# Kernel optimization log

Hardware: AMD Instinct MI355X
Metric: run time of the kernel (lower is better)

Reference implementation:

```python
import jax, jax.numpy as jnp
import numpy as np

N_NODES = 100000
N_EDGES = 1600000
F_IN = 16
F_OUT = 16
N_BASIS = 4  # per spatial dim; basisTerms = [4, 4]


def linear_basis(u, n):
    """Piecewise-linear (hat) basis, n terms on [-1, 1]. u: [E] -> [E, n]."""
    centers = jnp.linspace(-1.0, 1.0, n, dtype=u.dtype)
    dx = 2.0 / (n - 1)
    return jnp.maximum(0.0, 1.0 - jnp.abs(u[:, None] - centers[None, :]) / dx)


def setup_inputs() -> dict:
    key = jax.random.key(0)
    k1, k2, k3, k4, k5 = jax.random.split(key, 5)
    x = jax.random.normal(k1, (N_NODES, F_IN), dtype=jnp.float32)
    edge_index = jax.random.randint(k2, (2, N_EDGES), 0, N_NODES, dtype=jnp.int64)
    # relative positions normalized to [-1, 1]^2 (as in initializeWeights2D)
    edge_attr = jax.random.uniform(k3, (N_EDGES, 2), dtype=jnp.float32,
                                   minval=-1.0, maxval=1.0)
    # weight: [*basisTerms, inputFeatures, outputFeatures], uniform(-0.05, 0.05)
    weight = jax.random.uniform(k4, (N_BASIS, N_BASIS, F_IN, F_OUT),
                                dtype=jnp.float32, minval=-0.05, maxval=0.05)
    return {"x": x, "edge_index": edge_index, "edge_attr": edge_attr,
            "weight": weight}


def reference(x, edge_index, edge_attr, weight):
    """BasisConvLayer forward, mode='conv', linear basis, no bias/activations.

    For each edge e=(i<-j): msg_e = sum_{u,v} b_u(dx) b_v(dy) * (x_j @ W[u,v]);
    out[i] = sum over incoming edges of msg_e.
    """
    row, col = edge_index[0], edge_index[1]
    x_j = x[col]                                   # [E, F_in] gather
    bx = linear_basis(edge_attr[:, 0], N_BASIS)    # [E, nB]
    by = linear_basis(edge_attr[:, 1], N_BASIS)    # [E, nB]
    # outer product of 1D bases -> [E, nB*nB] interpolation coefficients
    t = (bx[:, :, None] * by[:, None, :]).reshape(-1, N_BASIS * N_BASIS)
    w_flat = weight.reshape(N_BASIS * N_BASIS, F_IN, F_OUT)
    # accumulate over the small fixed basis-term set to avoid [E, Fin, Fout]
    msg = jnp.zeros((x_j.shape[0], F_OUT), dtype=x.dtype)
    for k in range(N_BASIS * N_BASIS):
        msg = msg + t[:, k, None] * (x_j @ w_flat[k])
    out = jax.ops.segment_sum(msg, row, num_segments=N_NODES)  # scatter-add
    return out
```

## Files before the change

kernel.cpp:

```cpp
#include <hip/hip_runtime.h>

#define N_NODES 100000
#define N_EDGES 1600000
#define F 16

#define EDGES_PER_BLOCK 512
#define ITERS 4

#define OUT_FLOAT4 ((N_NODES * F) / 4)

typedef __attribute__((ext_vector_type(8))) short bf16x8;
typedef __attribute__((ext_vector_type(4))) float f32x4;

__global__ __launch_bounds__(256) void zero_out_kernel(float4* __restrict__ out) {
    int i = blockIdx.x * 256 + threadIdx.x;
    if (i < OUT_FLOAT4) out[i] = make_float4(0.f, 0.f, 0.f, 0.f);
}

__device__ __forceinline__ unsigned pk_bf16(float lo, float hi) {
    unsigned r;
    asm("v_cvt_pk_bf16_f32 %0, %1, %2" : "=v"(r) : "v"(lo), "v"(hi));
    return r;
}

__global__ __launch_bounds__(256, 4) void basis_conv_mfma(
    const float* __restrict__ x,
    const int*   __restrict__ edge_index,
    const float* __restrict__ edge_attr,
    const float* __restrict__ weight,
    float*       __restrict__ out)
{
    const int lane = threadIdx.x & 63;
    const int wid  = threadIdx.x >> 6;
    const int e15  = lane & 15;
    const int fo   = lane & 15;
    const int c    = lane >> 4;
    const int hv   = c >> 1;
    const int i0   = (c & 1) * 8;

    bf16x8 bw[8];
#pragma unroll
    for (int m = 0; m < 8; ++m) {
        const float* wp = weight + (2 * m + hv) * 256 + i0 * 16 + fo;
        union { bf16x8 v; unsigned w[4]; } bb;
#pragma unroll
        for (int p = 0; p < 4; ++p)
            bb.w[p] = pk_bf16(wp[(2 * p) * 16], wp[(2 * p + 1) * 16]);
        bw[m] = bb.v;
    }

    const int wbase = blockIdx.x * EDGES_PER_BLOCK + wid * (32 * ITERS);

    float2 at0[2], at1[2];
    int    col1[2];
    float4 xa0[2], xb0[2];

    {
#pragma unroll
        for (int u = 0; u < 2; ++u) {
            const int egA = wbase + u * 16;
            const int col0 = edge_index[N_EDGES + egA + e15];
            at0[u] = ((const float2*)edge_attr)[egA + e15];
            const float4* xv = (const float4*)(x + (size_t)col0 * 16 + i0);
            xa0[u] = xv[0]; xb0[u] = xv[1];
            const int egB = wbase + 32 + u * 16;
            col1[u] = edge_index[N_EDGES + egB + e15];
            at1[u]  = ((const float2*)edge_attr)[egB + e15];
        }
    }

#pragma unroll 1
    for (int g = 0; g < ITERS; ++g) {
        int4 r40[2];
#pragma unroll
        for (int u = 0; u < 2; ++u)
            r40[u] = *(const int4*)(edge_index + (wbase + g * 32 + u * 16) + 4 * c);

        float4 xa1[2], xb1[2];
#pragma unroll
        for (int u = 0; u < 2; ++u) {
            const float4* xv = (const float4*)(x + (size_t)col1[u] * 16 + i0);
            xa1[u] = xv[0]; xb1[u] = xv[1];
        }

        int col2[2]; float2 at2[2];
#pragma unroll
        for (int u = 0; u < 2; ++u) {
            int eg2 = wbase + (g + 2) * 32 + u * 16;
            eg2 = eg2 > (N_EDGES - 16) ? (N_EDGES - 16) : eg2;
            col2[u] = edge_index[N_EDGES + eg2 + e15];
            at2[u]  = ((const float2*)edge_attr)[eg2 + e15];
        }

        float bu_[2][4], bvE_[2], bvO_[2];
#pragma unroll
        for (int u = 0; u < 2; ++u) {
            float fu = (at0[u].x + 1.0f) * 1.5f;
            int iu = (int)fu; iu = iu < 0 ? 0 : (iu > 2 ? 2 : iu);
            const float wu1 = fu - (float)iu, wu0 = 1.0f - wu1;
            float fv = (at0[u].y + 1.0f) * 1.5f;
            int iv = (int)fv; iv = iv < 0 ? 0 : (iv > 2 ? 2 : iv);
            const float wv1 = fv - (float)iv, wv0 = 1.0f - wv1;

            bu_[u][0] = iu == 0 ? wu0 : 0.f;
            bu_[u][1] = iu == 0 ? wu1 : (iu == 1 ? wu0 : 0.f);
            bu_[u][2] = iu == 2 ? wu0 : (iu == 1 ? wu1 : 0.f);
            bu_[u][3] = iu == 2 ? wu1 : 0.f;
            const float bv0 = iv == 0 ? wv0 : 0.f;
            const float bv1 = iv == 0 ? wv1 : (iv == 1 ? wv0 : 0.f);
            const float bv2 = iv == 2 ? wv0 : (iv == 1 ? wv1 : 0.f);
            const float bv3 = iv == 2 ? wv1 : 0.f;
            bvE_[u] = hv ? bv1 : bv0;
            bvO_[u] = hv ? bv3 : bv2;
        }

        f32x4 accE[2] = {{0.f,0.f,0.f,0.f},{0.f,0.f,0.f,0.f}};
        f32x4 accO[2] = {{0.f,0.f,0.f,0.f},{0.f,0.f,0.f,0.f}};
#pragma unroll
        for (int m = 0; m < 8; ++m) {
#pragma unroll
            for (int u = 0; u < 2; ++u) {
                const float t = bu_[u][m >> 1] * ((m & 1) ? bvO_[u] : bvE_[u]);
                union { bf16x8 v; unsigned w[4]; } aa;
                aa.w[0] = pk_bf16(t * xa0[u].x, t * xa0[u].y);
                aa.w[1] = pk_bf16(t * xa0[u].z, t * xa0[u].w);
                aa.w[2] = pk_bf16(t * xb0[u].x, t * xb0[u].y);
                aa.w[3] = pk_bf16(t * xb0[u].z, t * xb0[u].w);
                if (m & 1)
                    accO[u] = __builtin_amdgcn_mfma_f32_16x16x32_bf16(aa.v, bw[m], accO[u], 0, 0, 0);
                else
                    accE[u] = __builtin_amdgcn_mfma_f32_16x16x32_bf16(aa.v, bw[m], accE[u], 0, 0, 0);
            }
        }

#pragma unroll
        for (int u = 0; u < 2; ++u) {
            const f32x4 acc = accE[u] + accO[u];
            unsafeAtomicAdd(out + (size_t)r40[u].x * 16 + fo, acc.x);
            unsafeAtomicAdd(out + (size_t)r40[u].y * 16 + fo, acc.y);
            unsafeAtomicAdd(out + (size_t)r40[u].z * 16 + fo, acc.z);
            unsafeAtomicAdd(out + (size_t)r40[u].w * 16 + fo, acc.w);
        }

#pragma unroll
        for (int u = 0; u < 2; ++u) {
            at0[u] = at1[u];
            xa0[u] = xa1[u]; xb0[u] = xb1[u];
            col1[u] = col2[u]; at1[u] = at2[u];
        }
    }
}

extern "C" void kernel_launch(void* const* d_in, const int* in_sizes, int n_in,
                              void* d_out, int out_size, void* d_ws, size_t ws_size,
                              hipStream_t stream) {
    const float* x  = (const float*)d_in[0];
    const int*   ei = (const int*)d_in[1];
    const float* ea = (const float*)d_in[2];
    const float* w  = (const float*)d_in[3];
    float* out = (float*)d_out;
    (void)out_size; (void)d_ws; (void)ws_size; (void)in_sizes; (void)n_in;

    zero_out_kernel<<<(OUT_FLOAT4 + 255) / 256, 256, 0, stream>>>((float4*)out);

    const int blocks = N_EDGES / EDGES_PER_BLOCK;
    basis_conv_mfma<<<blocks, 256, 0, stream>>>(x, ei, ea, w, out);
}
```

Baseline: 164.7 us.

## Accumulate scatter in bf16 workspace with packed bf16 atomics, then convert

The MFMA operands are swapped so each lane holds four consecutive output features of one edge. Those are packed to bf16 and scattered with two global_atomic_pk_add_bf16 per lane instead of four fp32 atomics. A bf16 workspace is zeroed first and expanded to fp32 output in an extra kernel. This halves atomic count and bytes, but accumulating about 16 edges per node in bf16 loses precision and may exceed tolerance, and the added launch costs some time.

```diff
diff --git a/kernel.cpp b/kernel.cpp
--- a/kernel.cpp
+++ b/kernel.cpp
@@ -7,14 +7,34 @@
 #define EDGES_PER_BLOCK 512
 #define ITERS 4
 
-#define OUT_FLOAT4 ((N_NODES * F) / 4)
+#define WS_ELEMS (N_NODES * F)
+#define WS_UINT4 (WS_ELEMS / 8)
+#define CVT_THREADS (WS_ELEMS / 8)
 
 typedef __attribute__((ext_vector_type(8))) short bf16x8;
 typedef __attribute__((ext_vector_type(4))) float f32x4;
 
-__global__ __launch_bounds__(256) void zero_out_kernel(float4* __restrict__ out) {
+__global__ __launch_bounds__(256) void zero_ws_kernel(uint4* __restrict__ ws) {
     int i = blockIdx.x * 256 + threadIdx.x;
-    if (i < OUT_FLOAT4) out[i] = make_float4(0.f, 0.f, 0.f, 0.f);
+    if (i < WS_UINT4) ws[i] = make_uint4(0u, 0u, 0u, 0u);
+}
+
+__global__ __launch_bounds__(256) void ws_to_out_kernel(const uint4* __restrict__ ws,
+                                                        float4* __restrict__ out) {
+    int i = blockIdx.x * 256 + threadIdx.x;
+    if (i >= CVT_THREADS) return;
+    const uint4 v = ws[i];
+    float4 a, b;
+    a.x = __builtin_bit_cast(float, v.x << 16);
+    a.y = __builtin_bit_cast(float, v.x & 0xffff0000u);
+    a.z = __builtin_bit_cast(float, v.y << 16);
+    a.w = __builtin_bit_cast(float, v.y & 0xffff0000u);
+    b.x = __builtin_bit_cast(float, v.z << 16);
+    b.y = __builtin_bit_cast(float, v.z & 0xffff0000u);
+    b.z = __builtin_bit_cast(float, v.w << 16);
+    b.w = __builtin_bit_cast(float, v.w & 0xffff0000u);
+    out[2 * i + 0] = a;
+    out[2 * i + 1] = b;
 }
 
 __device__ __forceinline__ unsigned pk_bf16(float lo, float hi) {
@@ -28,7 +48,7 @@
     const int*   __restrict__ edge_index,
     const float* __restrict__ edge_attr,
     const float* __restrict__ weight,
-    float*       __restrict__ out)
+    unsigned short* __restrict__ ws)
 {
     const int lane = threadIdx.x & 63;
     const int wid  = threadIdx.x >> 6;
@@ -54,7 +74,6 @@
     float2 at0[2], at1[2];
     int    col1[2];
     float4 xa0[2], xb0[2];
-
     {
 #pragma unroll
         for (int u = 0; u < 2; ++u) {
@@ -71,10 +90,10 @@
 
 #pragma unroll 1
     for (int g = 0; g < ITERS; ++g) {
-        int4 r40[2];
+        int rowd[2];
 #pragma unroll
         for (int u = 0; u < 2; ++u)
-            r40[u] = *(const int4*)(edge_index + (wbase + g * 32 + u * 16) + 4 * c);
+            rowd[u] = edge_index[wbase + g * 32 + u * 16 + e15];
 
         float4 xa1[2], xb1[2];
 #pragma unroll
@@ -127,19 +146,23 @@
                 aa.w[2] = pk_bf16(t * xb0[u].x, t * xb0[u].y);
                 aa.w[3] = pk_bf16(t * xb0[u].z, t * xb0[u].w);
                 if (m & 1)
-                    accO[u] = __builtin_amdgcn_mfma_f32_16x16x32_bf16(aa.v, bw[m], accO[u], 0, 0, 0);
+                    accO[u] = __builtin_amdgcn_mfma_f32_16x16x32_bf16(bw[m], aa.v, accO[u], 0, 0, 0);
                 else
-                    accE[u] = __builtin_amdgcn_mfma_f32_16x16x32_bf16(aa.v, bw[m], accE[u], 0, 0, 0);
+                    accE[u] = __builtin_amdgcn_mfma_f32_16x16x32_bf16(bw[m], aa.v, accE[u], 0, 0, 0);
             }
         }
 
 #pragma unroll
         for (int u = 0; u < 2; ++u) {
             const f32x4 acc = accE[u] + accO[u];
-            unsafeAtomicAdd(out + (size_t)r40[u].x * 16 + fo, acc.x);
-            unsafeAtomicAdd(out + (size_t)r40[u].y * 16 + fo, acc.y);
-            unsafeAtomicAdd(out + (size_t)r40[u].z * 16 + fo, acc.z);
-            unsafeAtomicAdd(out + (size_t)r40[u].w * 16 + fo, acc.w);
+            const unsigned d0 = pk_bf16(acc.x, acc.y);
+            const unsigned d1 = pk_bf16(acc.z, acc.w);
+            const unsigned long long a64 =
+                (unsigned long long)ws + (size_t)rowd[u] * 32 + c * 8;
+            asm volatile("global_atomic_pk_add_bf16 %0, %1, off"
+                         :: "v"(a64), "v"(d0) : "memory");
+            asm volatile("global_atomic_pk_add_bf16 %0, %1, off offset:4"
+                         :: "v"(a64), "v"(d1) : "memory");
         }
 
 #pragma unroll
@@ -159,10 +182,14 @@
     const float* ea = (const float*)d_in[2];
     const float* w  = (const float*)d_in[3];
     float* out = (float*)d_out;
-    (void)out_size; (void)d_ws; (void)ws_size; (void)in_sizes; (void)n_in;
+    unsigned short* ws = (unsigned short*)d_ws;
+    (void)out_size; (void)ws_size; (void)in_sizes; (void)n_in;
 
-    zero_out_kernel<<<(OUT_FLOAT4 + 255) / 256, 256, 0, stream>>>((float4*)out);
+    zero_ws_kernel<<<(WS_UINT4 + 255) / 256, 256, 0, stream>>>((uint4*)ws);
 
     const int blocks = N_EDGES / EDGES_PER_BLOCK;
-    basis_conv_mfma<<<blocks, 256, 0, stream>>>(x, ei, ea, w, out);
+    basis_conv_mfma<<<blocks, 256, 0, stream>>>(x, ei, ea, w, ws);
+
+    ws_to_out_kernel<<<(CVT_THREADS + 255) / 256, 256, 0, stream>>>(
+        (const uint4*)ws, (float4*)out);
 }
```

Result: slower. 244.8 us (+48.6%).

## Scatter via packed fixed-point 64-bit atomics with transposed MFMA output

Applied to the files above, without the earlier changes.

Swaps the MFMA operands so each lane holds four consecutive output features of one edge. Those four fp32 values are quantized to fixed-point int32 and packed in pairs into 64-bit integer atomics on a workspace, which halves the number of atomic operations per edge. A final kernel unpacks the workspace into float output. This adds two extra passes over a node-sized buffer and introduces quantization error and overflow risk from the fixed scale.

```diff
diff --git a/kernel.cpp b/kernel.cpp
--- a/kernel.cpp
+++ b/kernel.cpp
@@ -7,14 +7,27 @@
 #define EDGES_PER_BLOCK 512
 #define ITERS 4
 
-#define OUT_FLOAT4 ((N_NODES * F) / 4)
+#define WS_U64   (N_NODES * 8)
+#define WS_UINT4 (WS_U64 / 2)
+#define FP_SCALE 262144.0f
+#define FP_INV   (1.0f / 262144.0f)
 
 typedef __attribute__((ext_vector_type(8))) short bf16x8;
 typedef __attribute__((ext_vector_type(4))) float f32x4;
 
-__global__ __launch_bounds__(256) void zero_out_kernel(float4* __restrict__ out) {
+__global__ __launch_bounds__(256) void zero_ws_kernel(uint4* __restrict__ ws) {
     int i = blockIdx.x * 256 + threadIdx.x;
-    if (i < OUT_FLOAT4) out[i] = make_float4(0.f, 0.f, 0.f, 0.f);
+    if (i < WS_UINT4) ws[i] = make_uint4(0u, 0u, 0u, 0u);
+}
+
+__global__ __launch_bounds__(256) void ws_to_out_kernel(
+    const unsigned long long* __restrict__ ws, float2* __restrict__ out) {
+    int i = blockIdx.x * 256 + threadIdx.x;
+    if (i >= WS_U64) return;
+    const long long T = (long long)ws[i];
+    const int lo = (int)(unsigned)(T & 0xffffffffULL);
+    const int hi = (int)((T - (long long)lo) >> 32);
+    out[i] = make_float2((float)lo * FP_INV, (float)hi * FP_INV);
 }
 
 __device__ __forceinline__ unsigned pk_bf16(float lo, float hi) {
@@ -28,7 +41,7 @@
     const int*   __restrict__ edge_index,
     const float* __restrict__ edge_attr,
     const float* __restrict__ weight,
-    float*       __restrict__ out)
+    unsigned long long* __restrict__ ws)
 {
     const int lane = threadIdx.x & 63;
     const int wid  = threadIdx.x >> 6;
@@ -54,7 +67,6 @@
     float2 at0[2], at1[2];
     int    col1[2];
     float4 xa0[2], xb0[2];
-
     {
 #pragma unroll
         for (int u = 0; u < 2; ++u) {
@@ -71,10 +83,10 @@
 
 #pragma unroll 1
     for (int g = 0; g < ITERS; ++g) {
-        int4 r40[2];
+        int rowd[2];
 #pragma unroll
         for (int u = 0; u < 2; ++u)
-            r40[u] = *(const int4*)(edge_index + (wbase + g * 32 + u * 16) + 4 * c);
+            rowd[u] = edge_index[wbase + g * 32 + u * 16 + e15];
 
         float4 xa1[2], xb1[2];
 #pragma unroll
@@ -127,19 +139,22 @@
                 aa.w[2] = pk_bf16(t * xb0[u].x, t * xb0[u].y);
                 aa.w[3] = pk_bf16(t * xb0[u].z, t * xb0[u].w);
                 if (m & 1)
-                    accO[u] = __builtin_amdgcn_mfma_f32_16x16x32_bf16(aa.v, bw[m], accO[u], 0, 0, 0);
+                    accO[u] = __builtin_amdgcn_mfma_f32_16x16x32_bf16(bw[m], aa.v, accO[u], 0, 0, 0);
                 else
-                    accE[u] = __builtin_amdgcn_mfma_f32_16x16x32_bf16(aa.v, bw[m], accE[u], 0, 0, 0);
+                    accE[u] = __builtin_amdgcn_mfma_f32_16x16x32_bf16(bw[m], aa.v, accE[u], 0, 0, 0);
             }
         }
 
 #pragma unroll
         for (int u = 0; u < 2; ++u) {
             const f32x4 acc = accE[u] + accO[u];
-            unsafeAtomicAdd(out + (size_t)r40[u].x * 16 + fo, acc.x);
-            unsafeAtomicAdd(out + (size_t)r40[u].y * 16 + fo, acc.y);
-            unsafeAtomicAdd(out + (size_t)r40[u].z * 16 + fo, acc.z);
-            unsafeAtomicAdd(out + (size_t)r40[u].w * 16 + fo, acc.w);
+            const long long q0 = (long long)(int)(acc.x * FP_SCALE)
+                               + ((long long)(int)(acc.y * FP_SCALE) << 32);
+            const long long q1 = (long long)(int)(acc.z * FP_SCALE)
+                               + ((long long)(int)(acc.w * FP_SCALE) << 32);
+            unsigned long long* p = ws + (size_t)rowd[u] * 8 + c * 2;
+            atomicAdd(p,     (unsigned long long)q0);
+            atomicAdd(p + 1, (unsigned long long)q1);
         }
 
 #pragma unroll
@@ -159,10 +174,13 @@
     const float* ea = (const float*)d_in[2];
     const float* w  = (const float*)d_in[3];
     float* out = (float*)d_out;
-    (void)out_size; (void)d_ws; (void)ws_size; (void)in_sizes; (void)n_in;
+    unsigned long long* ws = (unsigned long long*)d_ws;
+    (void)out_size; (void)ws_size; (void)in_sizes; (void)n_in;
 
-    zero_out_kernel<<<(OUT_FLOAT4 + 255) / 256, 256, 0, stream>>>((float4*)out);
+    zero_ws_kernel<<<(WS_UINT4 + 255) / 256, 256, 0, stream>>>((uint4*)ws);
 
     const int blocks = N_EDGES / EDGES_PER_BLOCK;
-    basis_conv_mfma<<<blocks, 256, 0, stream>>>(x, ei, ea, w, out);
+    basis_conv_mfma<<<blocks, 256, 0, stream>>>(x, ei, ea, w, ws);
+
+    ws_to_out_kernel<<<(WS_U64 + 255) / 256, 256, 0, stream>>>(ws, (float2*)out);
 }
```

Result: slower. 226.5 us (+37.5%).

## Bucket edges by destination and reduce in LDS instead of global atomics

Applied to the files above, without the earlier changes.

Adds histogram, scan and scatter passes that group edges into buckets of 32 destination nodes, packing col, attributes and dest into a record array in workspace. The conv kernel then processes one bucket per block, accumulates messages with LDS atomics, and writes each output row once, which removes the zeroing pass and the per-element global float atomics. In exchange it adds extra launches, contended global atomics in the histogram and scatter, and extra memory traffic for writing and rereading the records.

```diff
diff --git a/kernel.cpp b/kernel.cpp
--- a/kernel.cpp
+++ b/kernel.cpp
@@ -4,18 +4,14 @@
 #define N_EDGES 1600000
 #define F 16
 
-#define EDGES_PER_BLOCK 512
-#define ITERS 4
-
-#define OUT_FLOAT4 ((N_NODES * F) / 4)
+#define NPB   32
+#define NB    3125
+#define NBPAD 3200
+
+#define REC_DW (N_EDGES * 4)
 
 typedef __attribute__((ext_vector_type(8))) short bf16x8;
 typedef __attribute__((ext_vector_type(4))) float f32x4;
-
-__global__ __launch_bounds__(256) void zero_out_kernel(float4* __restrict__ out) {
-    int i = blockIdx.x * 256 + threadIdx.x;
-    if (i < OUT_FLOAT4) out[i] = make_float4(0.f, 0.f, 0.f, 0.f);
-}
 
 __device__ __forceinline__ unsigned pk_bf16(float lo, float hi) {
     unsigned r;
@@ -23,13 +19,70 @@
     return r;
 }
 
-__global__ __launch_bounds__(256, 4) void basis_conv_mfma(
+__global__ __launch_bounds__(256) void zero_hist_kernel(unsigned* __restrict__ hist) {
+    int i = blockIdx.x * 256 + threadIdx.x;
+    if (i < NBPAD) hist[i] = 0u;
+}
+
+__global__ __launch_bounds__(256) void hist_kernel(const int* __restrict__ ei,
+                                                   unsigned* __restrict__ hist) {
+    const int stride = gridDim.x * 256;
+    for (int e = blockIdx.x * 256 + threadIdx.x; e < N_EDGES; e += stride)
+        atomicAdd(&hist[((unsigned)ei[e]) >> 5], 1u);
+}
+
+__global__ __launch_bounds__(1024) void scan_kernel(const unsigned* __restrict__ hist,
+                                                    unsigned* __restrict__ offs,
+                                                    unsigned* __restrict__ cur) {
+    __shared__ unsigned lds[1024];
+    const int t = threadIdx.x;
+    unsigned c[4]; unsigned s = 0;
+#pragma unroll
+    for (int k = 0; k < 4; ++k) {
+        const int b = t * 4 + k;
+        c[k] = (b < NB) ? hist[b] : 0u;
+        s += c[k];
+    }
+    lds[t] = s;
+    __syncthreads();
+    for (int off = 1; off < 1024; off <<= 1) {
+        unsigned v = (t >= off) ? lds[t - off] : 0u;
+        __syncthreads();
+        lds[t] += v;
+        __syncthreads();
+    }
+    unsigned run = (t == 0) ? 0u : lds[t - 1];
+#pragma unroll
+    for (int k = 0; k < 4; ++k) {
+        const int b = t * 4 + k;
+        if (b < NB) { offs[b] = run; cur[b] = run; run += c[k]; }
+    }
+    if (t == 1023) offs[NB] = run;
+}
+
+__global__ __launch_bounds__(256) void scatter_kernel(const int* __restrict__ ei,
+                                                      const float2* __restrict__ attr,
+                                                      unsigned* __restrict__ cur,
+                                                      float4* __restrict__ rec) {
+    const int stride = gridDim.x * 256;
+    for (int e = blockIdx.x * 256 + threadIdx.x; e < N_EDGES; e += stride) {
+        const int dest = ei[e];
+        const int col  = ei[N_EDGES + e];
+        const float2 a = attr[e];
+        const unsigned p = atomicAdd(&cur[((unsigned)dest) >> 5], 1u);
+        rec[p] = make_float4(__int_as_float(col), a.x, a.y, __int_as_float(dest));
+    }
+}
+
+__global__ __launch_bounds__(256, 4) void conv_bucket(
     const float* __restrict__ x,
-    const int*   __restrict__ edge_index,
-    const float* __restrict__ edge_attr,
+    const float4* __restrict__ rec,
+    const unsigned* __restrict__ offs,
     const float* __restrict__ weight,
-    float*       __restrict__ out)
+    float* __restrict__ out)
 {
+    __shared__ float accs[NPB * F];
+
     const int lane = threadIdx.x & 63;
     const int wid  = threadIdx.x >> 6;
     const int e15  = lane & 15;
@@ -49,56 +102,42 @@
         bw[m] = bb.v;
     }
 
-    const int wbase = blockIdx.x * EDGES_PER_BLOCK + wid * (32 * ITERS);
-
-    float2 at0[2], at1[2];
-    int    col1[2];
-    float4 xa0[2], xb0[2];
-
-    {
-#pragma unroll
-        for (int u = 0; u < 2; ++u) {
-            const int egA = wbase + u * 16;
-            const int col0 = edge_index[N_EDGES + egA + e15];
-            at0[u] = ((const float2*)edge_attr)[egA + e15];
-            const float4* xv = (const float4*)(x + (size_t)col0 * 16 + i0);
-            xa0[u] = xv[0]; xb0[u] = xv[1];
-            const int egB = wbase + 32 + u * 16;
-            col1[u] = edge_index[N_EDGES + egB + e15];
-            at1[u]  = ((const float2*)edge_attr)[egB + e15];
-        }
-    }
-
-#pragma unroll 1
-    for (int g = 0; g < ITERS; ++g) {
-        int4 r40[2];
-#pragma unroll
-        for (int u = 0; u < 2; ++u)
-            r40[u] = *(const int4*)(edge_index + (wbase + g * 32 + u * 16) + 4 * c);
-
-        float4 xa1[2], xb1[2];
-#pragma unroll
-        for (int u = 0; u < 2; ++u) {
-            const float4* xv = (const float4*)(x + (size_t)col1[u] * 16 + i0);
-            xa1[u] = xv[0]; xb1[u] = xv[1];
-        }
-
-        int col2[2]; float2 at2[2];
-#pragma unroll
-        for (int u = 0; u < 2; ++u) {
-            int eg2 = wbase + (g + 2) * 32 + u * 16;
-            eg2 = eg2 > (N_EDGES - 16) ? (N_EDGES - 16) : eg2;
-            col2[u] = edge_index[N_EDGES + eg2 + e15];
-            at2[u]  = ((const float2*)edge_attr)[eg2 + e15];
+    const int b    = blockIdx.x;
+    const int base = b * NPB;
+    const unsigned start = offs[b];
+    const unsigned end   = offs[b + 1];
+
+    for (int i = threadIdx.x; i < NPB * F; i += 256) accs[i] = 0.f;
+    __syncthreads();
+
+    for (unsigned eb = start + wid * 32; eb < end; eb += 128) {
+        int   ln[2]; float vm[2]; float2 at[2]; int col[2];
+#pragma unroll
+        for (int u = 0; u < 2; ++u) {
+            const unsigned idx = eb + u * 16 + e15;
+            const bool valid = idx < end;
+            const float4 r = rec[valid ? idx : start];
+            col[u] = __float_as_int(r.x);
+            at[u]  = make_float2(r.y, r.z);
+            const int local = (__float_as_int(r.w) - base) & (NPB - 1);
+            ln[u] = valid ? local : 0;
+            vm[u] = valid ? 1.f : 0.f;
+        }
+
+        float4 xa[2], xb[2];
+#pragma unroll
+        for (int u = 0; u < 2; ++u) {
+            const float4* xv = (const float4*)(x + (size_t)col[u] * 16 + i0);
+            xa[u] = xv[0]; xb[u] = xv[1];
         }
 
         float bu_[2][4], bvE_[2], bvO_[2];
 #pragma unroll
         for (int u = 0; u < 2; ++u) {
-            float fu = (at0[u].x + 1.0f) * 1.5f;
+            float fu = (at[u].x + 1.0f) * 1.5f;
             int iu = (int)fu; iu = iu < 0 ? 0 : (iu > 2 ? 2 : iu);
             const float wu1 = fu - (float)iu, wu0 = 1.0f - wu1;
-            float fv = (at0[u].y + 1.0f) * 1.5f;
+            float fv = (at[u].y + 1.0f) * 1.5f;
             int iv = (int)fv; iv = iv < 0 ? 0 : (iv > 2 ? 2 : iv);
             const float wv1 = fv - (float)iv, wv0 = 1.0f - wv1;
 
@@ -110,8 +149,8 @@
             const float bv1 = iv == 0 ? wv1 : (iv == 1 ? wv0 : 0.f);
             const float bv2 = iv == 2 ? wv0 : (iv == 1 ? wv1 : 0.f);
             const float bv3 = iv == 2 ? wv1 : 0.f;
-            bvE_[u] = hv ? bv1 : bv0;
-            bvO_[u] = hv ? bv3 : bv2;
+            bvE_[u] = (hv ? bv1 : bv0) * vm[u];
+            bvO_[u] = (hv ? bv3 : bv2) * vm[u];
         }
 
         f32x4 accE[2] = {{0.f,0.f,0.f,0.f},{0.f,0.f,0.f,0.f}};
@@ -122,33 +161,31 @@
             for (int u = 0; u < 2; ++u) {
                 const float t = bu_[u][m >> 1] * ((m & 1) ? bvO_[u] : bvE_[u]);
                 union { bf16x8 v; unsigned w[4]; } aa;
-                aa.w[0] = pk_bf16(t * xa0[u].x, t * xa0[u].y);
-                aa.w[1] = pk_bf16(t * xa0[u].z, t * xa0[u].w);
-                aa.w[2] = pk_bf16(t * xb0[u].x, t * xb0[u].y);
-                aa.w[3] = pk_bf16(t * xb0[u].z, t * xb0[u].w);
+                aa.w[0] = pk_bf16(t * xa[u].x, t * xa[u].y);
+                aa.w[1] = pk_bf16(t * xa[u].z, t * xa[u].w);
+                aa.w[2] = pk_bf16(t * xb[u].x, t * xb[u].y);
+                aa.w[3] = pk_bf16(t * xb[u].z, t * xb[u].w);
                 if (m & 1)
-                    accO[u] = __builtin_amdgcn_mfma_f32_16x16x32_bf16(aa.v, bw[m], accO[u], 0, 0, 0);
+                    accO[u] = __builtin_amdgcn_mfma_f32_16x16x32_bf16(bw[m], aa.v, accO[u], 0, 0, 0);
                 else
-                    accE[u] = __builtin_amdgcn_mfma_f32_16x16x32_bf16(aa.v, bw[m], accE[u], 0, 0, 0);
+                    accE[u] = __builtin_amdgcn_mfma_f32_16x16x32_bf16(bw[m], aa.v, accE[u], 0, 0, 0);
             }
         }
 
 #pragma unroll
         for (int u = 0; u < 2; ++u) {
             const f32x4 acc = accE[u] + accO[u];
-            unsafeAtomicAdd(out + (size_t)r40[u].x * 16 + fo, acc.x);
-            unsafeAtomicAdd(out + (size_t)r40[u].y * 16 + fo, acc.y);
-            unsafeAtomicAdd(out + (size_t)r40[u].z * 16 + fo, acc.z);
-            unsafeAtomicAdd(out + (size_t)r40[u].w * 16 + fo, acc.w);
-        }
-
-#pragma unroll
-        for (int u = 0; u < 2; ++u) {
-            at0[u] = at1[u];
-            xa0[u] = xa1[u]; xb0[u] = xb1[u];
-            col1[u] = col2[u]; at1[u] = at2[u];
-        }
-    }
+            float* p = &accs[ln[u] * F + c * 4];
+            atomicAdd(p + 0, acc.x);
+            atomicAdd(p + 1, acc.y);
+            atomicAdd(p + 2, acc.z);
+            atomicAdd(p + 3, acc.w);
+        }
+    }
+
+    __syncthreads();
+    for (int i = threadIdx.x; i < NPB * F; i += 256)
+        out[(size_t)base * F + i] = accs[i];
 }
 
 extern "C" void kernel_launch(void* const* d_in, const int* in_sizes, int n_in,
@@ -159,10 +196,16 @@
     const float* ea = (const float*)d_in[2];
     const float* w  = (const float*)d_in[3];
     float* out = (float*)d_out;
-    (void)out_size; (void)d_ws; (void)ws_size; (void)in_sizes; (void)n_in;
-
-    zero_out_kernel<<<(OUT_FLOAT4 + 255) / 256, 256, 0, stream>>>((float4*)out);
-
-    const int blocks = N_EDGES / EDGES_PER_BLOCK;
-    basis_conv_mfma<<<blocks, 256, 0, stream>>>(x, ei, ea, w, out);
-}
+    (void)out_size; (void)ws_size; (void)in_sizes; (void)n_in;
+
+    float4*   rec  = (float4*)d_ws;
+    unsigned* hist = (unsigned*)d_ws + REC_DW;
+    unsigned* offs = hist + NBPAD;
+    unsigned* cur  = offs + NBPAD;
+
+    zero_hist_kernel<<<(NBPAD + 255) / 256, 256, 0, stream>>>(hist);
+    hist_kernel<<<2048, 256, 0, stream>>>(ei, hist);
+    scan_kernel<<<1, 1024, 0, stream>>>(hist, offs, cur);
+    scatter_kernel<<<2048, 256, 0, stream>>>(ei, (const float2*)ea, cur, rec);
+    conv_bucket<<<NB, 256, 0, stream>>>(x, rec, offs, w, out);
+}
```

Result: slower. 505.8 us (+207.1%).
